# Optimization experiments

Measured on AMD Instinct MI355X. Metric: run time of the kernel, lower is better.

The kernel has to match this reference:

```python
import jax, jax.numpy as jnp
import numpy as np

NUM_EXPERTS = 8

def setup_inputs() -> dict:
    key = jax.random.key(0)
    k1, k2, k3, k4, k5 = jax.random.split(key, 5)
    T, D, H, O, E, K = 4096, 1024, 2048, 1024, NUM_EXPERTS, 2
    hidden_states = jax.random.normal(k1, (T, D), dtype=jnp.float32)
    top_k_indices = jax.random.randint(k2, (T, K), 0, E, dtype=jnp.int64)
    top_k_weights = jax.random.uniform(k3, (T, K), dtype=jnp.float32)
    gate_up_proj = jax.random.normal(k4, (E, 2 * H, D), dtype=jnp.float32) * 0.02
    down_proj = jax.random.normal(k5, (E, O, H), dtype=jnp.float32) * 0.02
    return {
        "hidden_states": hidden_states,
        "top_k_indices": top_k_indices,
        "top_k_weights": top_k_weights,
        "gate_up_proj": gate_up_proj,
        "down_proj": down_proj,
    }


def _moe(hidden_states, top_k_weights, gate_up_proj, down_proj, top_k_indices):
    # Mathematically identical to the torch per-token-gather loop, expressed as
    # dense all-expert compute + sparse combine (non-selected experts get weight 0).
    T = hidden_states.shape[0]
    E = gate_up_proj.shape[0]
    # [T, E, 2H]
    gate_up = jnp.einsum('td,ehd->teh', hidden_states, gate_up_proj)
    gate, up = jnp.split(gate_up, 2, axis=-1)
    h = jax.nn.silu(gate) * up  # [T, E, H]
    expert_out = jnp.einsum('teh,eoh->teo', h, down_proj)  # [T, E, O]
    # combine weights: scatter top-k routing weights into [T, E]
    combine = jnp.zeros((T, E), dtype=hidden_states.dtype)
    rows = jnp.arange(T)[:, None]
    combine = combine.at[rows, top_k_indices].add(top_k_weights)
    return jnp.einsum('teo,te->to', expert_out, combine)


def reference(hidden_states, top_k_indices, top_k_weights, gate_up_proj, down_proj):
    return _moe(hidden_states, top_k_weights, gate_up_proj, down_proj, top_k_indices)
```

## Files before the change

kernel.cpp:

```cpp
#include <hip/hip_runtime.h>
#include <stdint.h>

#define TOKS 4096
#define DIM  1024
#define HID  2048
#define OUTD 1024
#define NE   8
#define MP   9216
#define NBR  72

typedef __bf16 bf16;
typedef bf16 bf16x8 __attribute__((ext_vector_type(8)));
typedef float f32x4 __attribute__((ext_vector_type(4)));
typedef __attribute__((address_space(1))) void gvoid;
typedef __attribute__((address_space(3))) void lvoid;

#define WGU_OFF  0ull
#define WD_OFF   (WGU_OFF + 67108864ull)
#define XG_OFF   (WD_OFF  + 33554432ull)
#define H_OFF    (XG_OFF  + 18874368ull)
#define TK_OFF   (H_OFF   + 37748736ull)
#define META_OFF (TK_OFF  + 36864ull)
#define T2S_OFF  (META_OFF + 1024ull)

__device__ __forceinline__ unsigned short f2bf(float f) {
  union { float f; unsigned u; } v; v.f = f;
  unsigned r = (v.u + 0x7FFFu + ((v.u >> 16) & 1u)) >> 16;
  return (unsigned short)r;
}
__device__ __forceinline__ unsigned pack2(float a, float b) {
  return (unsigned)f2bf(a) | ((unsigned)f2bf(b) << 16);
}
__device__ __forceinline__ void cp16(const void* g, void* l) {
  __builtin_amdgcn_global_load_lds((gvoid*)(void*)g, (lvoid*)l, 16, 0, 0);
}

__global__ __launch_bounds__(1024) void route_kernel(const int* __restrict__ idx,
                                                     int* __restrict__ table,
                                                     int* __restrict__ slot_token,
                                                     int* __restrict__ tok2slot) {
  __shared__ int cnt[NE], offs[NE], cur[NE];
  const int tid = threadIdx.x, lane = tid & 63;
  for (int i = tid; i < MP; i += 1024) slot_token[i] = -1;
  if (tid < NE) cnt[tid] = 0;
  __syncthreads();
  int myE[8];
#pragma unroll
  for (int c = 0; c < 8; ++c) myE[c] = idx[c * 1024 + tid];
#pragma unroll
  for (int c = 0; c < 8; ++c) {
    int e = myE[c];
#pragma unroll
    for (int ex = 0; ex < NE; ++ex) {
      unsigned long long m = __ballot(e == ex);
      if (lane == 0 && m) atomicAdd(&cnt[ex], __popcll(m));
    }
  }
  __syncthreads();
  if (tid == 0) {
    int cum = 0;
    for (int e = 0; e < NE; ++e) {
      offs[e] = cum; cur[e] = 0;
      int nb = (cnt[e] + 127) >> 7;
      int bb = cum >> 7;
      for (int b = 0; b < nb; ++b) table[bb + b] = e;
      cum += nb << 7;
    }
    for (int b = cum >> 7; b < NBR; ++b) table[b] = -1;
  }
  __syncthreads();
#pragma unroll
  for (int c = 0; c < 8; ++c) {
    int e = myE[c];
    int pos = 0;
#pragma unroll
    for (int ex = 0; ex < NE; ++ex) {
      unsigned long long m = __ballot(e == ex);
      if (e == ex) {
        int rank = __popcll(m & ((1ull << lane) - 1ull));
        int leader = __ffsll(m) - 1;
        int base = 0;
        if (lane == leader) base = atomicAdd(&cur[ex], __popcll(m));
        base = __shfl(base, leader);
        pos = offs[ex] + base + rank;
      }
    }
    slot_token[pos] = (c * 1024 + tid) >> 1;
    tok2slot[c * 1024 + tid] = pos;
  }
}

__global__ void gather_kernel(const float* __restrict__ X, const int* __restrict__ slot_token,
                              uint4* __restrict__ Xg) {
  int gid = blockIdx.x * 256 + threadIdx.x;
  int row = gid >> 7, j = (gid & 127) << 3;
  int t = slot_token[row];
  uint4 o;
  if (t >= 0) {
    const float4* p = (const float4*)(X + (size_t)t * DIM + j);
    float4 a = p[0], b = p[1];
    o.x = pack2(a.x, a.y); o.y = pack2(a.z, a.w);
    o.z = pack2(b.x, b.y); o.w = pack2(b.z, b.w);
  } else {
    o = uint4{0u, 0u, 0u, 0u};
  }
  Xg[gid] = o;
}

__global__ void convert_kernel(const float4* __restrict__ srcGu, uint2* __restrict__ dstGu,
                               const float4* __restrict__ srcD, uint2* __restrict__ dstD) {
  const int n1 = NE * 2 * HID * DIM / 4;
  int i = blockIdx.x * 256 + threadIdx.x;
  float4 v; uint2* dp;
  if (i < n1) { v = srcGu[i]; dp = dstGu + i; }
  else        { v = srcD[i - n1]; dp = dstD + (i - n1); }
  uint2 o; o.x = pack2(v.x, v.y); o.y = pack2(v.z, v.w);
  *dp = o;
}

__global__ void combine_kernel(const float* __restrict__ Obuf, const int* __restrict__ tok2slot,
                               const float* __restrict__ wts, float4* __restrict__ out) {
  int t = blockIdx.x, c = threadIdx.x;
  int s0 = tok2slot[2 * t], s1 = tok2slot[2 * t + 1];
  float w0 = wts[2 * t], w1 = wts[2 * t + 1];
  float4 a = ((const float4*)(Obuf + (size_t)s0 * OUTD))[c];
  float4 b = ((const float4*)(Obuf + (size_t)s1 * OUTD))[c];
  out[(size_t)t * (OUTD / 4) + c] =
      float4{w0 * a.x + w1 * b.x, w0 * a.y + w1 * b.y, w0 * a.z + w1 * b.z, w0 * a.w + w1 * b.w};
}

__global__ __launch_bounds__(256) void gemm1_kernel(
    const unsigned short* __restrict__ Xg,
    const unsigned short* __restrict__ Wgu,
    unsigned short* __restrict__ Hbuf,
    const int* __restrict__ table) {
  int e = table[blockIdx.y];
  if (e < 0) return;
  const int tid = threadIdx.x;
  const int lane = tid & 63, wave = tid >> 6;
  const int wm = wave >> 1, wn = wave & 1;
  const int lr = lane & 15, quad = lane >> 4;

  __shared__ bf16 As[128 * 64];
  __shared__ bf16 Bg[64 * 64];
  __shared__ bf16 Bu[64 * 64];

  const unsigned short* A_base  = Xg  + (size_t)blockIdx.y * 128 * DIM;
  const unsigned short* Wg_base = Wgu + (size_t)e * 2 * HID * DIM + (size_t)(blockIdx.x * 64) * DIM;
  const unsigned short* Wu_base = Wg_base + (size_t)HID * DIM;

  f32x4 accg[4][2] = {}; f32x4 accu[4][2] = {};

  for (int kt = 0; kt < DIM / 64; ++kt) {
    const int kb = kt * 64;
#pragma unroll
    for (int i = 0; i < 4; ++i) {
      int s = i * 256 + tid, row = s >> 3, pc = s & 7, gc = pc ^ (row & 7);
      cp16(A_base + (size_t)row * DIM + kb + gc * 8, (void*)(As + row * 64 + pc * 8));
    }
#pragma unroll
    for (int i = 0; i < 2; ++i) {
      int s = i * 256 + tid, row = s >> 3, pc = s & 7, gc = pc ^ (row & 7);
      cp16(Wg_base + (size_t)row * DIM + kb + gc * 8, (void*)(Bg + row * 64 + pc * 8));
      cp16(Wu_base + (size_t)row * DIM + kb + gc * 8, (void*)(Bu + row * 64 + pc * 8));
    }
    __syncthreads();
#pragma unroll
    for (int ks = 0; ks < 2; ++ks) {
      bf16x8 a[4], bg[2], bu[2];
#pragma unroll
      for (int i = 0; i < 4; ++i) {
        int row = wm * 64 + i * 16 + lr;
        int pc = (ks * 4 + quad) ^ (row & 7);
        a[i] = *(const bf16x8*)(As + row * 64 + pc * 8);
      }
#pragma unroll
      for (int j = 0; j < 2; ++j) {
        int row = wn * 32 + j * 16 + lr;
        int pc = (ks * 4 + quad) ^ (row & 7);
        bg[j] = *(const bf16x8*)(Bg + row * 64 + pc * 8);
        bu[j] = *(const bf16x8*)(Bu + row * 64 + pc * 8);
      }
#pragma unroll
      for (int i = 0; i < 4; ++i)
#pragma unroll
        for (int j = 0; j < 2; ++j) {
          accg[i][j] = __builtin_amdgcn_mfma_f32_16x16x32_bf16(a[i], bg[j], accg[i][j], 0, 0, 0);
          accu[i][j] = __builtin_amdgcn_mfma_f32_16x16x32_bf16(a[i], bu[j], accu[i][j], 0, 0, 0);
        }
    }
    __syncthreads();
  }

  const int rowBase = blockIdx.y * 128 + wm * 64;
  const int colBase = blockIdx.x * 64 + wn * 32;
#pragma unroll
  for (int i = 0; i < 4; ++i)
#pragma unroll
    for (int r = 0; r < 4; ++r) {
      int row = rowBase + i * 16 + quad * 4 + r;
#pragma unroll
      for (int j = 0; j < 2; ++j) {
        float g = accg[i][j][r], u = accu[i][j][r];
        float s = g / (1.0f + __expf(-g));
        Hbuf[(size_t)row * HID + colBase + j * 16 + lr] = f2bf(s * u);
      }
    }
}

__global__ __launch_bounds__(256) void gemm2_kernel(
    const unsigned short* __restrict__ Hbuf,
    const unsigned short* __restrict__ Wd,
    float* __restrict__ Obuf,
    const int* __restrict__ table) {
  int e = table[blockIdx.y];
  if (e < 0) return;
  const int tid = threadIdx.x;
  const int lane = tid & 63, wave = tid >> 6;
  const int wm = wave >> 1, wn = wave & 1;
  const int lr = lane & 15, quad = lane >> 4;

  __shared__ bf16 As[128 * 64];
  __shared__ bf16 Bs[128 * 64];

  const unsigned short* A_base = Hbuf + (size_t)blockIdx.y * 128 * HID;
  const unsigned short* B_base = Wd + (size_t)e * OUTD * HID + (size_t)(blockIdx.x * 128) * HID;

  f32x4 acc[4][4] = {};

  for (int kt = 0; kt < HID / 64; ++kt) {
    const int kb = kt * 64;
#pragma unroll
    for (int i = 0; i < 4; ++i) {
      int s = i * 256 + tid, row = s >> 3, pc = s & 7, gc = pc ^ (row & 7);
      cp16(A_base + (size_t)row * HID + kb + gc * 8, (void*)(As + row * 64 + pc * 8));
      cp16(B_base + (size_t)row * HID + kb + gc * 8, (void*)(Bs + row * 64 + pc * 8));
    }
    __syncthreads();
#pragma unroll
    for (int ks = 0; ks < 2; ++ks) {
      bf16x8 a[4], b[4];
#pragma unroll
      for (int i = 0; i < 4; ++i) {
        int row = wm * 64 + i * 16 + lr;
        int pc = (ks * 4 + quad) ^ (row & 7);
        a[i] = *(const bf16x8*)(As + row * 64 + pc * 8);
      }
#pragma unroll
      for (int j = 0; j < 4; ++j) {
        int row = wn * 64 + j * 16 + lr;
        int pc = (ks * 4 + quad) ^ (row & 7);
        b[j] = *(const bf16x8*)(Bs + row * 64 + pc * 8);
      }
#pragma unroll
      for (int i = 0; i < 4; ++i)
#pragma unroll
        for (int j = 0; j < 4; ++j)
          acc[i][j] = __builtin_amdgcn_mfma_f32_16x16x32_bf16(a[i], b[j], acc[i][j], 0, 0, 0);
    }
    __syncthreads();
  }

  const int rowBase = blockIdx.y * 128 + wm * 64;
  const int colBase = blockIdx.x * 128 + wn * 64;
#pragma unroll
  for (int i = 0; i < 4; ++i)
#pragma unroll
    for (int r = 0; r < 4; ++r) {
      int row = rowBase + i * 16 + quad * 4 + r;
      float* Orow = Obuf + (size_t)row * OUTD + colBase;
#pragma unroll
      for (int j = 0; j < 4; ++j)
        Orow[j * 16 + lr] = acc[i][j][r];
    }
}

extern "C" void kernel_launch(void* const* d_in, const int* in_sizes, int n_in,
                              void* d_out, int out_size, void* d_ws, size_t ws_size,
                              hipStream_t stream) {
  const float* X     = (const float*)d_in[0];
  const int*   idx   = (const int*)d_in[1];
  const float* wts   = (const float*)d_in[2];
  const float* WguF  = (const float*)d_in[3];
  const float* WdF   = (const float*)d_in[4];
  float* out = (float*)d_out;

  char* base = (char*)d_ws;
  unsigned short* Wgu = (unsigned short*)(base + WGU_OFF);
  unsigned short* Wd  = (unsigned short*)(base + WD_OFF);
  unsigned short* Xg  = (unsigned short*)(base + XG_OFF);
  unsigned short* Hb  = (unsigned short*)(base + H_OFF);
  float* Obuf         = (float*)(base + WGU_OFF);
  int*   slot_token = (int*)(base + TK_OFF);
  int*   table      = (int*)(base + META_OFF);
  int*   tok2slot   = (int*)(base + T2S_OFF);

  route_kernel<<<1, 1024, 0, stream>>>(idx, table, slot_token, tok2slot);
  gather_kernel<<<(MP * 128) / 256, 256, 0, stream>>>(X, slot_token, (uint4*)Xg);
  {
    const int nTot = (NE * 2 * HID * DIM + NE * OUTD * HID) / 4;
    convert_kernel<<<nTot / 256, 256, 0, stream>>>((const float4*)WguF, (uint2*)Wgu,
                                                   (const float4*)WdF, (uint2*)Wd);
  }
  gemm1_kernel<<<dim3(HID / 64, NBR), 256, 0, stream>>>(Xg, Wgu, Hb, table);
  gemm2_kernel<<<dim3(OUTD / 128, NBR), 256, 0, stream>>>(Hb, Wd, Obuf, table);
  combine_kernel<<<TOKS, 256, 0, stream>>>(Obuf, tok2slot, wts, (float4*)out);
}
```

Baseline: 438.6 us.

## Split-K gemm2 into two bf16 partial buffers and fuse gather with weight conversion

Merges the gather and weight-conversion kernels into one launch. Splits the down-projection GEMM's K dimension in two, doubling the grid from 8x72 to 8x72x2 blocks so it fills more compute units. Each half writes bf16 partials that the combine kernel sums. This trades extra rounding (bf16 partials instead of fp32 output) for better occupancy of gemm2 and less write and read traffic.

```diff
diff --git a/kernel.cpp b/kernel.cpp
--- a/kernel.cpp
+++ b/kernel.cpp
@@ -22,11 +22,16 @@
 #define TK_OFF   (H_OFF   + 37748736ull)
 #define META_OFF (TK_OFF  + 36864ull)
 #define T2S_OFF  (META_OFF + 1024ull)
+#define O0_OFF   WGU_OFF
+#define O1_OFF   (WGU_OFF + 18874368ull)
 
 __device__ __forceinline__ unsigned short f2bf(float f) {
   union { float f; unsigned u; } v; v.f = f;
   unsigned r = (v.u + 0x7FFFu + ((v.u >> 16) & 1u)) >> 16;
   return (unsigned short)r;
+}
+__device__ __forceinline__ float bf2f(unsigned short h) {
+  union { unsigned u; float f; } v; v.u = ((unsigned)h) << 16; return v.f;
 }
 __device__ __forceinline__ unsigned pack2(float a, float b) {
   return (unsigned)f2bf(a) | ((unsigned)f2bf(b) << 16);
@@ -90,43 +95,54 @@
   }
 }
 
-__global__ void gather_kernel(const float* __restrict__ X, const int* __restrict__ slot_token,
-                              uint4* __restrict__ Xg) {
-  int gid = blockIdx.x * 256 + threadIdx.x;
-  int row = gid >> 7, j = (gid & 127) << 3;
-  int t = slot_token[row];
-  uint4 o;
-  if (t >= 0) {
-    const float4* p = (const float4*)(X + (size_t)t * DIM + j);
-    float4 a = p[0], b = p[1];
-    o.x = pack2(a.x, a.y); o.y = pack2(a.z, a.w);
-    o.z = pack2(b.x, b.y); o.w = pack2(b.z, b.w);
+#define GATHER_B 4608
+__global__ void prep_kernel(const float* __restrict__ X, const int* __restrict__ slot_token,
+                            uint4* __restrict__ Xg,
+                            const float4* __restrict__ srcGu, uint2* __restrict__ dstGu,
+                            const float4* __restrict__ srcD, uint2* __restrict__ dstD) {
+  int bx = blockIdx.x;
+  if (bx < GATHER_B) {
+    int gid = bx * 256 + threadIdx.x;
+    int row = gid >> 7, j = (gid & 127) << 3;
+    int t = slot_token[row];
+    uint4 o;
+    if (t >= 0) {
+      const float4* p = (const float4*)(X + (size_t)t * DIM + j);
+      float4 a = p[0], b = p[1];
+      o.x = pack2(a.x, a.y); o.y = pack2(a.z, a.w);
+      o.z = pack2(b.x, b.y); o.w = pack2(b.z, b.w);
+    } else {
+      o = uint4{0u, 0u, 0u, 0u};
+    }
+    Xg[gid] = o;
   } else {
-    o = uint4{0u, 0u, 0u, 0u};
-  }
-  Xg[gid] = o;
-}
-
-__global__ void convert_kernel(const float4* __restrict__ srcGu, uint2* __restrict__ dstGu,
-                               const float4* __restrict__ srcD, uint2* __restrict__ dstD) {
-  const int n1 = NE * 2 * HID * DIM / 4;
-  int i = blockIdx.x * 256 + threadIdx.x;
-  float4 v; uint2* dp;
-  if (i < n1) { v = srcGu[i]; dp = dstGu + i; }
-  else        { v = srcD[i - n1]; dp = dstD + (i - n1); }
-  uint2 o; o.x = pack2(v.x, v.y); o.y = pack2(v.z, v.w);
-  *dp = o;
-}
-
-__global__ void combine_kernel(const float* __restrict__ Obuf, const int* __restrict__ tok2slot,
+    const int n1 = NE * 2 * HID * DIM / 4;
+    int i = (bx - GATHER_B) * 256 + threadIdx.x;
+    float4 v; uint2* dp;
+    if (i < n1) { v = srcGu[i]; dp = dstGu + i; }
+    else        { v = srcD[i - n1]; dp = dstD + (i - n1); }
+    uint2 o; o.x = pack2(v.x, v.y); o.y = pack2(v.z, v.w);
+    *dp = o;
+  }
+}
+
+__global__ void combine_kernel(const unsigned short* __restrict__ O0,
+                               const unsigned short* __restrict__ O1,
+                               const int* __restrict__ tok2slot,
                                const float* __restrict__ wts, float4* __restrict__ out) {
   int t = blockIdx.x, c = threadIdx.x;
   int s0 = tok2slot[2 * t], s1 = tok2slot[2 * t + 1];
   float w0 = wts[2 * t], w1 = wts[2 * t + 1];
-  float4 a = ((const float4*)(Obuf + (size_t)s0 * OUTD))[c];
-  float4 b = ((const float4*)(Obuf + (size_t)s1 * OUTD))[c];
-  out[(size_t)t * (OUTD / 4) + c] =
-      float4{w0 * a.x + w1 * b.x, w0 * a.y + w1 * b.y, w0 * a.z + w1 * b.z, w0 * a.w + w1 * b.w};
+  uint2 a0 = ((const uint2*)(O0 + (size_t)s0 * OUTD))[c];
+  uint2 b0 = ((const uint2*)(O1 + (size_t)s0 * OUTD))[c];
+  uint2 a1 = ((const uint2*)(O0 + (size_t)s1 * OUTD))[c];
+  uint2 b1 = ((const uint2*)(O1 + (size_t)s1 * OUTD))[c];
+  float4 o;
+  o.x = w0 * (bf2f(a0.x & 0xFFFF) + bf2f(b0.x & 0xFFFF)) + w1 * (bf2f(a1.x & 0xFFFF) + bf2f(b1.x & 0xFFFF));
+  o.y = w0 * (bf2f(a0.x >> 16)    + bf2f(b0.x >> 16))    + w1 * (bf2f(a1.x >> 16)    + bf2f(b1.x >> 16));
+  o.z = w0 * (bf2f(a0.y & 0xFFFF) + bf2f(b0.y & 0xFFFF)) + w1 * (bf2f(a1.y & 0xFFFF) + bf2f(b1.y & 0xFFFF));
+  o.w = w0 * (bf2f(a0.y >> 16)    + bf2f(b0.y >> 16))    + w1 * (bf2f(a1.y >> 16)    + bf2f(b1.y >> 16));
+  out[(size_t)t * (OUTD / 4) + c] = o;
 }
 
 __global__ __launch_bounds__(256) void gemm1_kernel(
@@ -211,7 +227,8 @@
 __global__ __launch_bounds__(256) void gemm2_kernel(
     const unsigned short* __restrict__ Hbuf,
     const unsigned short* __restrict__ Wd,
-    float* __restrict__ Obuf,
+    unsigned short* __restrict__ O0,
+    unsigned short* __restrict__ O1,
     const int* __restrict__ table) {
   int e = table[blockIdx.y];
   if (e < 0) return;
@@ -219,16 +236,18 @@
   const int lane = tid & 63, wave = tid >> 6;
   const int wm = wave >> 1, wn = wave & 1;
   const int lr = lane & 15, quad = lane >> 4;
+  const int kslice = blockIdx.z;
 
   __shared__ bf16 As[128 * 64];
   __shared__ bf16 Bs[128 * 64];
 
-  const unsigned short* A_base = Hbuf + (size_t)blockIdx.y * 128 * HID;
-  const unsigned short* B_base = Wd + (size_t)e * OUTD * HID + (size_t)(blockIdx.x * 128) * HID;
+  const unsigned short* A_base = Hbuf + (size_t)blockIdx.y * 128 * HID + kslice * (HID / 2);
+  const unsigned short* B_base = Wd + (size_t)e * OUTD * HID + (size_t)(blockIdx.x * 128) * HID
+                               + kslice * (HID / 2);
 
   f32x4 acc[4][4] = {};
 
-  for (int kt = 0; kt < HID / 64; ++kt) {
+  for (int kt = 0; kt < (HID / 2) / 64; ++kt) {
     const int kb = kt * 64;
 #pragma unroll
     for (int i = 0; i < 4; ++i) {
@@ -261,6 +280,7 @@
     __syncthreads();
   }
 
+  unsigned short* O = kslice ? O1 : O0;
   const int rowBase = blockIdx.y * 128 + wm * 64;
   const int colBase = blockIdx.x * 128 + wn * 64;
 #pragma unroll
@@ -268,10 +288,10 @@
 #pragma unroll
     for (int r = 0; r < 4; ++r) {
       int row = rowBase + i * 16 + quad * 4 + r;
-      float* Orow = Obuf + (size_t)row * OUTD + colBase;
+      unsigned short* Orow = O + (size_t)row * OUTD + colBase;
 #pragma unroll
       for (int j = 0; j < 4; ++j)
-        Orow[j * 16 + lr] = acc[i][j][r];
+        Orow[j * 16 + lr] = f2bf(acc[i][j][r]);
     }
 }
 
@@ -290,19 +310,19 @@
   unsigned short* Wd  = (unsigned short*)(base + WD_OFF);
   unsigned short* Xg  = (unsigned short*)(base + XG_OFF);
   unsigned short* Hb  = (unsigned short*)(base + H_OFF);
-  float* Obuf         = (float*)(base + WGU_OFF);
-  int*   slot_token = (int*)(base + TK_OFF);
-  int*   table      = (int*)(base + META_OFF);
-  int*   tok2slot   = (int*)(base + T2S_OFF);
+  unsigned short* O0  = (unsigned short*)(base + O0_OFF);
+  unsigned short* O1  = (unsigned short*)(base + O1_OFF);
+  int* slot_token = (int*)(base + TK_OFF);
+  int* table      = (int*)(base + META_OFF);
+  int* tok2slot   = (int*)(base + T2S_OFF);
 
   route_kernel<<<1, 1024, 0, stream>>>(idx, table, slot_token, tok2slot);
-  gather_kernel<<<(MP * 128) / 256, 256, 0, stream>>>(X, slot_token, (uint4*)Xg);
   {
-    const int nTot = (NE * 2 * HID * DIM + NE * OUTD * HID) / 4;
-    convert_kernel<<<nTot / 256, 256, 0, stream>>>((const float4*)WguF, (uint2*)Wgu,
-                                                   (const float4*)WdF, (uint2*)Wd);
+    const int convB = (NE * 2 * HID * DIM + NE * OUTD * HID) / 4 / 256;
+    prep_kernel<<<GATHER_B + convB, 256, 0, stream>>>(X, slot_token, (uint4*)Xg,
+        (const float4*)WguF, (uint2*)Wgu, (const float4*)WdF, (uint2*)Wd);
   }
   gemm1_kernel<<<dim3(HID / 64, NBR), 256, 0, stream>>>(Xg, Wgu, Hb, table);
-  gemm2_kernel<<<dim3(OUTD / 128, NBR), 256, 0, stream>>>(Hb, Wd, Obuf, table);
-  combine_kernel<<<TOKS, 256, 0, stream>>>(Obuf, tok2slot, wts, (float4*)out);
-}
+  gemm2_kernel<<<dim3(OUTD / 128, NBR, 2), 256, 0, stream>>>(Hb, Wd, O0, O1, table);
+  combine_kernel<<<TOKS, 256, 0, stream>>>(O0, O1, tok2slot, wts, (float4*)out);
+}
```

New measurement: 435.8 us. About the same (-0.7%).
